# Kernel tuning notes

Measured on AMD Instinct MI355X. Metric: run time of the kernel, lower is better.

Reference implementation:

```python
import jax, jax.numpy as jnp
import numpy as np
from jax import lax

ITER_TIME = 32
DECAY = 0.9


def setup_inputs() -> dict:
    key = jax.random.key(0)
    k1, k2, k3, k4 = jax.random.split(key, 4)
    B, D_in, N, D_out = 256, 1024, 4096, 256
    s_in = 1.0 / np.sqrt(D_in)
    s_rec = 0.5 / np.sqrt(N)  # keep recurrence stable
    s_out = 1.0 / np.sqrt(N)
    return {
        "x": jax.random.normal(k1, (B, D_in), dtype=jnp.float32),
        "W_i": jax.random.normal(k2, (D_in, N), dtype=jnp.float32) * s_in,
        "b": jnp.zeros((N,), dtype=jnp.float32),
        "W_r": jax.random.normal(k3, (N, N), dtype=jnp.float32) * s_rec,
        "W_f": jax.random.normal(k4, (N, D_out), dtype=jnp.float32) * s_out,
    }


def reference(x, W_i, b, W_r, W_f):
    # prep_input_endure: constant input drive each timestep
    i_ = x @ W_i + b  # [B, N]
    u0 = jnp.zeros_like(i_)
    r0 = jnp.zeros_like(i_)

    def step(carry, _):
        u, r = carry
        u_new = DECAY * u + i_ + r           # leaky integration of drive + recurrent feedback
        a = jax.nn.relu(u_new)               # firing rate / surrogate spike
        r_new = a @ W_r                      # recurrent N->N feedback
        f = a @ W_f                          # readout N->Y
        return (u_new, r_new), (f, u_new)

    (_, _), (fs, us) = lax.scan(step, (u0, r0), None, length=ITER_TIME)
    output = jnp.transpose(fs, (1, 0, 2))  # [B, T, output_num]
    act = jnp.transpose(us, (1, 0, 2))     # [B, T, N_num]
    return output, act
```

## Files before the change

kernel.cpp:

```cpp
#include <hip/hip_runtime.h>
#include <hip/hip_bf16.h>

#define ITER_TIME 32
#define DECAY 0.9f

typedef __attribute__((ext_vector_type(8))) short short8;
typedef __attribute__((ext_vector_type(4))) float f32x4;
typedef __attribute__((ext_vector_type(4))) short short4v;
typedef unsigned short ushort_t;
typedef unsigned int u32;

__device__ __forceinline__ void gload16(const ushort_t* g, ushort_t* l) {
    __builtin_amdgcn_global_load_lds(
        (const __attribute__((address_space(1))) u32*)g,
        (__attribute__((address_space(3))) u32*)l, 16, 0, 0);
}

__global__ void conv_f32_bf16(const float* __restrict__ in,
                              __hip_bfloat16* __restrict__ out, int n) {
    int i = blockIdx.x * 256 + threadIdx.x;
    if (i < n) out[i] = __float2bfloat16(in[i]);
}

__global__ void transpose_f32_bf16(const float* __restrict__ in,
                                   __hip_bfloat16* __restrict__ out, int R,
                                   int C) {
    __shared__ float tile[32][33];
    int tx = threadIdx.x, ty = threadIdx.y;
    size_t x = blockIdx.x * 32 + tx;
    size_t y = blockIdx.y * 32 + ty;
    tile[ty][tx] = in[y * C + x];
    __syncthreads();
    size_t ox = blockIdx.y * 32 + tx;
    size_t oy = blockIdx.x * 32 + ty;
    out[oy * R + ox] = __float2bfloat16(tile[tx][ty]);
}

__global__ __launch_bounds__(256)
void gemm_splitk(const ushort_t* __restrict__ A,
                 const ushort_t* __restrict__ BT,
                 const ushort_t* __restrict__ BT2,
                 float* __restrict__ Cp,
                 float* __restrict__ C2p,
                 int K, int klen, int Nmain, int N2) {
    const int M = 256;
    __shared__ __attribute__((aligned(16))) ushort_t As[2][128 * 64];
    __shared__ __attribute__((aligned(16))) ushort_t Bs[2][128 * 64];

    int m0 = blockIdx.x * 128;
    int by = blockIdx.y;
    int ks = blockIdx.z;
    int ntile_main = Nmain >> 7;
    bool isB2 = (by >= ntile_main);
    const ushort_t* Bsrc = isB2 ? BT2 + (size_t)((by - ntile_main) * 128) * K
                                : BT + (size_t)(by * 128) * K;

    int t = threadIdx.x;
    int wave = t >> 6, lane = t & 63;
    int quad = lane >> 4, l16 = lane & 15;
    int wm = (wave >> 1) * 64, wn = (wave & 1) * 64;

    int lr = lane >> 3;
    int lcol = ((lane & 7) ^ lr) << 3;
    const ushort_t* aBase = A + (size_t)(m0 + wave * 32 + lr) * K + lcol;
    const ushort_t* bBase = Bsrc + (size_t)(wave * 32 + lr) * K + lcol;

    f32x4 acc[4][4];
#pragma unroll
    for (int i = 0; i < 4; i++)
#pragma unroll
        for (int j = 0; j < 4; j++) acc[i][j] = (f32x4){0.f, 0.f, 0.f, 0.f};

    int k0 = ks * klen;
    int nt = klen >> 6;

    int swz = (l16 & 7) << 3;

    auto stage = [&](int buf, int kk) {
#pragma unroll
        for (int i = 0; i < 4; ++i) {
            gload16(aBase + (size_t)(i * 8) * K + kk,
                    &As[buf][(wave * 4 + i) * 512]);
            gload16(bBase + (size_t)(i * 8) * K + kk,
                    &Bs[buf][(wave * 4 + i) * 512]);
        }
    };

    stage(0, k0);
    __syncthreads();
    int cur = 0;
    for (int it = 0; it < nt; ++it) {
        if (it + 1 < nt) stage(cur ^ 1, k0 + (it + 1) * 64);
#pragma unroll
        for (int kstep = 0; kstep < 2; ++kstep) {
            int ko = kstep * 32 + quad * 8;
            int pc = ko ^ swz;
            short8 af[4], bfr[4];
#pragma unroll
            for (int i = 0; i < 4; i++)
                af[i] = *(const short8*)&As[cur][(wm + i * 16 + l16) * 64 + pc];
#pragma unroll
            for (int j = 0; j < 4; j++)
                bfr[j] = *(const short8*)&Bs[cur][(wn + j * 16 + l16) * 64 + pc];
#pragma unroll
            for (int i = 0; i < 4; i++)
#pragma unroll
                for (int j = 0; j < 4; j++)
                    acc[i][j] = __builtin_amdgcn_mfma_f32_16x16x32_bf16(
                        af[i], bfr[j], acc[i][j], 0, 0, 0);
        }
        __syncthreads();
        cur ^= 1;
    }

#pragma unroll
    for (int i = 0; i < 4; i++) {
#pragma unroll
        for (int j = 0; j < 4; j++) {
            int gcol = by * 128 + wn + j * 16 + l16;
#pragma unroll
            for (int rr = 0; rr < 4; ++rr) {
                int grow = m0 + wm + i * 16 + quad * 4 + rr;
                float v = acc[i][j][rr];
                if (!isB2) {
                    Cp[(size_t)ks * M * Nmain + (size_t)grow * Nmain + gcol] = v;
                } else {
                    int c2 = gcol - Nmain;
                    C2p[(size_t)ks * M * N2 + (size_t)grow * N2 + c2] = v;
                }
            }
        }
    }
}

__global__ void elem_step(float* __restrict__ i_, float* __restrict__ u,
                          __hip_bfloat16* __restrict__ a,
                          const float* __restrict__ rp,
                          const float* __restrict__ fp,
                          const float* __restrict__ bias,
                          float* __restrict__ out, float* __restrict__ act,
                          int t, int KS) {
    int id4 = blockIdx.x * 256 + threadIdx.x;
    const int NU = 256 * 4096;
    const int NU4 = NU / 4;
    if (id4 < NU4) {
        if (t >= ITER_TIME) return;
        int id = id4 * 4;
        int b = id >> 12, n = id & 4095;
        f32x4 un;
        if (t == 0) {
            f32x4 iv = *(f32x4*)&i_[id] + *(const f32x4*)&bias[n];
            *(f32x4*)&i_[id] = iv;
            un = iv;
        } else {
            f32x4 s = *(f32x4*)&i_[id];
            for (int k = 0; k < KS; ++k)
                s += *(const f32x4*)&rp[(size_t)k * NU + id];
            un = DECAY * *(f32x4*)&u[id] + s;
        }
        *(f32x4*)&u[id] = un;
        short4v av;
#pragma unroll
        for (int j = 0; j < 4; ++j) {
            float ar = un[j] > 0.f ? un[j] : 0.f;
            __hip_bfloat16 h = __float2bfloat16(ar);
            av[j] = *(short*)&h;
        }
        *(short4v*)&a[id] = av;
        *(f32x4*)&act[(size_t)b * (ITER_TIME * 4096) + (size_t)t * 4096 + n] =
            un;
    } else {
        if (t == 0) return;
        int id2 = (id4 - NU4) * 4;
        const int NF = 256 * 256;
        int b = id2 >> 8, d = id2 & 255;
        f32x4 fv = {0.f, 0.f, 0.f, 0.f};
        for (int k = 0; k < KS; ++k)
            fv += *(const f32x4*)&fp[(size_t)k * NF + id2];
        *(f32x4*)&out[(size_t)b * (ITER_TIME * 256) + (size_t)(t - 1) * 256 +
                      d] = fv;
    }
}

extern "C" void kernel_launch(void* const* d_in, const int* in_sizes, int n_in,
                              void* d_out, int out_size, void* d_ws,
                              size_t ws_size, hipStream_t stream) {
    const float* x = (const float*)d_in[0];
    const float* Wi = (const float*)d_in[1];
    const float* bb = (const float*)d_in[2];
    const float* Wr = (const float*)d_in[3];
    const float* Wf = (const float*)d_in[4];

    float* out = (float*)d_out;
    float* act = out + (size_t)256 * ITER_TIME * 256;

    int KS = 8;
    if (ws_size < (size_t)0x4E80000) KS = 4;

    char* ws = (char*)d_ws;
    float* i_ = (float*)(ws + 0x0);
    float* u = (float*)(ws + 0x400000);
    __hip_bfloat16* a = (__hip_bfloat16*)(ws + 0x800000);
    size_t off = 0xA00000;
    float* rp = (float*)(ws + off);
    off += (size_t)KS << 22;
    float* fp = (float*)(ws + off);
    off += (size_t)KS << 18;
    __hip_bfloat16* WrT = (__hip_bfloat16*)(ws + off);
    off += 0x2000000;
    __hip_bfloat16* WfT = (__hip_bfloat16*)(ws + off);
    off += 0x200000;
    __hip_bfloat16* xb = (__hip_bfloat16*)(ws + off);
    __hip_bfloat16* WiT = (__hip_bfloat16*)(ws + 0xA00000);

    conv_f32_bf16<<<1024, 256, 0, stream>>>(x, xb, 256 * 1024);
    dim3 tb(32, 32);
    transpose_f32_bf16<<<dim3(128, 32), tb, 0, stream>>>(Wi, WiT, 1024, 4096);
    transpose_f32_bf16<<<dim3(128, 128), tb, 0, stream>>>(Wr, WrT, 4096, 4096);
    transpose_f32_bf16<<<dim3(8, 128), tb, 0, stream>>>(Wf, WfT, 4096, 256);

    gemm_splitk<<<dim3(2, 32, 1), 256, 0, stream>>>(
        (const ushort_t*)xb, (const ushort_t*)WiT, nullptr, i_, nullptr, 1024,
        1024, 4096, 256);

    int klen = 4096 / KS;
    for (int t = 0; t <= ITER_TIME; ++t) {
        elem_step<<<1088, 256, 0, stream>>>(i_, u, a, rp, fp, bb, out, act, t,
                                            KS);
        if (t < ITER_TIME) {
            gemm_splitk<<<dim3(2, 34, KS), 256, 0, stream>>>(
                (const ushort_t*)a, (const ushort_t*)WrT,
                (const ushort_t*)WfT, rp, fp, 4096, klen, 4096, 256);
        }
    }
}
```

Measured before the change: 1.337 ms.

## Fuse recurrent timestep loop into one persistent kernel with grid barriers

Replaces the 65 per-timestep launches of the elementwise and split-K GEMM kernels with a single persistent kernel of 272 blocks. The blocks alternate the elementwise update and the GEMM tiles, separated by atomic-counter grid barriers. Split-K is fixed at 4, and the act/out stores become nontemporal. This removes launch overhead and inter-kernel gaps, but relies on all 272 blocks being co-resident (otherwise it deadlocks) and adds spin-wait barrier cost.

```diff
diff --git a/kernel.cpp b/kernel.cpp
--- a/kernel.cpp
+++ b/kernel.cpp
@@ -3,6 +3,8 @@
 
 #define ITER_TIME 32
 #define DECAY 0.9f
+#define KS 4
+#define NBLK 272
 
 typedef __attribute__((ext_vector_type(8))) short short8;
 typedef __attribute__((ext_vector_type(4))) float f32x4;
@@ -17,7 +19,9 @@
 }
 
 __global__ void conv_f32_bf16(const float* __restrict__ in,
-                              __hip_bfloat16* __restrict__ out, int n) {
+                              __hip_bfloat16* __restrict__ out, int n,
+                              int* __restrict__ bar) {
+    if (blockIdx.x == 0 && threadIdx.x == 0) *bar = 0;
     int i = blockIdx.x * 256 + threadIdx.x;
     if (i < n) out[i] = __float2bfloat16(in[i]);
 }
@@ -37,23 +41,16 @@
 }
 
 __global__ __launch_bounds__(256)
-void gemm_splitk(const ushort_t* __restrict__ A,
-                 const ushort_t* __restrict__ BT,
-                 const ushort_t* __restrict__ BT2,
-                 float* __restrict__ Cp,
-                 float* __restrict__ C2p,
-                 int K, int klen, int Nmain, int N2) {
-    const int M = 256;
+void gemm_wi(const ushort_t* __restrict__ A,
+             const ushort_t* __restrict__ BT,
+             float* __restrict__ C,
+             int K, int Nmain) {
     __shared__ __attribute__((aligned(16))) ushort_t As[2][128 * 64];
     __shared__ __attribute__((aligned(16))) ushort_t Bs[2][128 * 64];
 
     int m0 = blockIdx.x * 128;
     int by = blockIdx.y;
-    int ks = blockIdx.z;
-    int ntile_main = Nmain >> 7;
-    bool isB2 = (by >= ntile_main);
-    const ushort_t* Bsrc = isB2 ? BT2 + (size_t)((by - ntile_main) * 128) * K
-                                : BT + (size_t)(by * 128) * K;
+    const ushort_t* Bsrc = BT + (size_t)(by * 128) * K;
 
     int t = threadIdx.x;
     int wave = t >> 6, lane = t & 63;
@@ -71,9 +68,7 @@
 #pragma unroll
         for (int j = 0; j < 4; j++) acc[i][j] = (f32x4){0.f, 0.f, 0.f, 0.f};
 
-    int k0 = ks * klen;
-    int nt = klen >> 6;
-
+    int nt = K >> 6;
     int swz = (l16 & 7) << 3;
 
     auto stage = [&](int buf, int kk) {
@@ -86,11 +81,11 @@
         }
     };
 
-    stage(0, k0);
+    stage(0, 0);
     __syncthreads();
     int cur = 0;
     for (int it = 0; it < nt; ++it) {
-        if (it + 1 < nt) stage(cur ^ 1, k0 + (it + 1) * 64);
+        if (it + 1 < nt) stage(cur ^ 1, (it + 1) * 64);
 #pragma unroll
         for (int kstep = 0; kstep < 2; ++kstep) {
             int ko = kstep * 32 + quad * 8;
@@ -114,7 +109,163 @@
     }
 
 #pragma unroll
-    for (int i = 0; i < 4; i++) {
+    for (int i = 0; i < 4; i++)
+#pragma unroll
+        for (int j = 0; j < 4; j++) {
+            int gcol = by * 128 + wn + j * 16 + l16;
+#pragma unroll
+            for (int rr = 0; rr < 4; ++rr) {
+                int grow = m0 + wm + i * 16 + quad * 4 + rr;
+                C[(size_t)grow * Nmain + gcol] = acc[i][j][rr];
+            }
+        }
+}
+
+__device__ __forceinline__ void grid_bar(int* bar, int phase) {
+    __syncthreads();
+    if (threadIdx.x == 0) {
+        __threadfence();
+        __hip_atomic_fetch_add(bar, 1, __ATOMIC_RELEASE,
+                               __HIP_MEMORY_SCOPE_AGENT);
+        int target = NBLK * (phase + 1);
+        while (__hip_atomic_load(bar, __ATOMIC_ACQUIRE,
+                                 __HIP_MEMORY_SCOPE_AGENT) < target)
+            __builtin_amdgcn_s_sleep(2);
+    }
+    __syncthreads();
+}
+
+__device__ __forceinline__ void elem_work(int t, float* __restrict__ i_,
+                                          float* __restrict__ u,
+                                          ushort_t* __restrict__ a,
+                                          const float* __restrict__ rp,
+                                          const float* __restrict__ fp,
+                                          const float* __restrict__ bias,
+                                          float* __restrict__ out,
+                                          float* __restrict__ act) {
+    const int NU = 256 * 4096, NU4 = NU / 4;
+    const int NF = 256 * 256, NF4 = NF / 4;
+    int gtid = blockIdx.x * 256 + threadIdx.x;
+    for (int id4 = gtid; id4 < NU4 + NF4; id4 += NBLK * 256) {
+        if (id4 < NU4) {
+            if (t >= ITER_TIME) continue;
+            int id = id4 * 4;
+            int b = id >> 12, n = id & 4095;
+            f32x4 un;
+            if (t == 0) {
+                f32x4 iv = *(f32x4*)&i_[id] + *(const f32x4*)&bias[n];
+                *(f32x4*)&i_[id] = iv;
+                un = iv;
+            } else {
+                f32x4 s = *(const f32x4*)&i_[id];
+#pragma unroll
+                for (int k = 0; k < KS; ++k)
+                    s += *(const f32x4*)&rp[(size_t)k * NU + id];
+                un = DECAY * *(f32x4*)&u[id] + s;
+            }
+            *(f32x4*)&u[id] = un;
+            short4v av;
+#pragma unroll
+            for (int j = 0; j < 4; ++j) {
+                float ar = un[j] > 0.f ? un[j] : 0.f;
+                __hip_bfloat16 h = __float2bfloat16(ar);
+                av[j] = *(short*)&h;
+            }
+            *(short4v*)&a[id] = av;
+            __builtin_nontemporal_store(
+                un, (f32x4*)&act[(size_t)b * (ITER_TIME * 4096) +
+                                 (size_t)t * 4096 + n]);
+        } else {
+            if (t == 0) continue;
+            int id2 = (id4 - NU4) * 4;
+            int b = id2 >> 8, d = id2 & 255;
+            f32x4 fv = {0.f, 0.f, 0.f, 0.f};
+#pragma unroll
+            for (int k = 0; k < KS; ++k)
+                fv += *(const f32x4*)&fp[(size_t)k * NF + id2];
+            __builtin_nontemporal_store(
+                fv, (f32x4*)&out[(size_t)b * (ITER_TIME * 256) +
+                                 (size_t)(t - 1) * 256 + d]);
+        }
+    }
+}
+
+__device__ __forceinline__ void gemm_tile(int blk, const ushort_t* __restrict__ A,
+                                          const ushort_t* __restrict__ WrT,
+                                          const ushort_t* __restrict__ WfT,
+                                          float* __restrict__ rp,
+                                          float* __restrict__ fp,
+                                          ushort_t* __restrict__ AsB,
+                                          ushort_t* __restrict__ BsB) {
+    const int K = 4096, klen = K / KS, Nmain = 4096, N2 = 256, M = 256;
+    int rem = blk % 68, ks = blk / 68;
+    int mt = rem & 1, by = rem >> 1;
+    int m0 = mt * 128;
+    bool isB2 = (by >= 32);
+    const ushort_t* Bsrc = isB2 ? WfT + (size_t)((by - 32) * 128) * K
+                                : WrT + (size_t)(by * 128) * K;
+
+    int t = threadIdx.x;
+    int wave = t >> 6, lane = t & 63;
+    int quad = lane >> 4, l16 = lane & 15;
+    int wm = (wave >> 1) * 64, wn = (wave & 1) * 64;
+
+    int lr = lane >> 3;
+    int lcol = ((lane & 7) ^ lr) << 3;
+    const ushort_t* aBase = A + (size_t)(m0 + wave * 32 + lr) * K + lcol;
+    const ushort_t* bBase = Bsrc + (size_t)(wave * 32 + lr) * K + lcol;
+
+    f32x4 acc[4][4];
+#pragma unroll
+    for (int i = 0; i < 4; i++)
+#pragma unroll
+        for (int j = 0; j < 4; j++) acc[i][j] = (f32x4){0.f, 0.f, 0.f, 0.f};
+
+    int k0 = ks * klen;
+    const int nt = klen >> 6;
+    int swz = (l16 & 7) << 3;
+
+    auto stage = [&](int buf, int kk) {
+#pragma unroll
+        for (int i = 0; i < 4; ++i) {
+            gload16(aBase + (size_t)(i * 8) * K + kk,
+                    &AsB[buf * 8192 + (wave * 4 + i) * 512]);
+            gload16(bBase + (size_t)(i * 8) * K + kk,
+                    &BsB[buf * 8192 + (wave * 4 + i) * 512]);
+        }
+    };
+
+    stage(0, k0);
+    __syncthreads();
+    int cur = 0;
+    for (int it = 0; it < nt; ++it) {
+        if (it + 1 < nt) stage(cur ^ 1, k0 + (it + 1) * 64);
+#pragma unroll
+        for (int kstep = 0; kstep < 2; ++kstep) {
+            int ko = kstep * 32 + quad * 8;
+            int pc = ko ^ swz;
+            short8 af[4], bfr[4];
+#pragma unroll
+            for (int i = 0; i < 4; i++)
+                af[i] = *(const short8*)&AsB[cur * 8192 +
+                                             (wm + i * 16 + l16) * 64 + pc];
+#pragma unroll
+            for (int j = 0; j < 4; j++)
+                bfr[j] = *(const short8*)&BsB[cur * 8192 +
+                                              (wn + j * 16 + l16) * 64 + pc];
+#pragma unroll
+            for (int i = 0; i < 4; i++)
+#pragma unroll
+                for (int j = 0; j < 4; j++)
+                    acc[i][j] = __builtin_amdgcn_mfma_f32_16x16x32_bf16(
+                        af[i], bfr[j], acc[i][j], 0, 0, 0);
+        }
+        __syncthreads();
+        cur ^= 1;
+    }
+
+#pragma unroll
+    for (int i = 0; i < 4; i++)
 #pragma unroll
         for (int j = 0; j < 4; j++) {
             int gcol = by * 128 + wn + j * 16 + l16;
@@ -123,63 +274,33 @@
                 int grow = m0 + wm + i * 16 + quad * 4 + rr;
                 float v = acc[i][j][rr];
                 if (!isB2) {
-                    Cp[(size_t)ks * M * Nmain + (size_t)grow * Nmain + gcol] = v;
+                    rp[(size_t)ks * M * Nmain + (size_t)grow * Nmain + gcol] = v;
                 } else {
                     int c2 = gcol - Nmain;
-                    C2p[(size_t)ks * M * N2 + (size_t)grow * N2 + c2] = v;
+                    fp[(size_t)ks * M * N2 + (size_t)grow * N2 + c2] = v;
                 }
             }
         }
-    }
-}
-
-__global__ void elem_step(float* __restrict__ i_, float* __restrict__ u,
-                          __hip_bfloat16* __restrict__ a,
-                          const float* __restrict__ rp,
-                          const float* __restrict__ fp,
-                          const float* __restrict__ bias,
-                          float* __restrict__ out, float* __restrict__ act,
-                          int t, int KS) {
-    int id4 = blockIdx.x * 256 + threadIdx.x;
-    const int NU = 256 * 4096;
-    const int NU4 = NU / 4;
-    if (id4 < NU4) {
-        if (t >= ITER_TIME) return;
-        int id = id4 * 4;
-        int b = id >> 12, n = id & 4095;
-        f32x4 un;
-        if (t == 0) {
-            f32x4 iv = *(f32x4*)&i_[id] + *(const f32x4*)&bias[n];
-            *(f32x4*)&i_[id] = iv;
-            un = iv;
-        } else {
-            f32x4 s = *(f32x4*)&i_[id];
-            for (int k = 0; k < KS; ++k)
-                s += *(const f32x4*)&rp[(size_t)k * NU + id];
-            un = DECAY * *(f32x4*)&u[id] + s;
-        }
-        *(f32x4*)&u[id] = un;
-        short4v av;
-#pragma unroll
-        for (int j = 0; j < 4; ++j) {
-            float ar = un[j] > 0.f ? un[j] : 0.f;
-            __hip_bfloat16 h = __float2bfloat16(ar);
-            av[j] = *(short*)&h;
-        }
-        *(short4v*)&a[id] = av;
-        *(f32x4*)&act[(size_t)b * (ITER_TIME * 4096) + (size_t)t * 4096 + n] =
-            un;
-    } else {
-        if (t == 0) return;
-        int id2 = (id4 - NU4) * 4;
-        const int NF = 256 * 256;
-        int b = id2 >> 8, d = id2 & 255;
-        f32x4 fv = {0.f, 0.f, 0.f, 0.f};
-        for (int k = 0; k < KS; ++k)
-            fv += *(const f32x4*)&fp[(size_t)k * NF + id2];
-        *(f32x4*)&out[(size_t)b * (ITER_TIME * 256) + (size_t)(t - 1) * 256 +
-                      d] = fv;
-    }
+}
+
+__global__ __launch_bounds__(256, 2)
+void persist(ushort_t* __restrict__ a, const ushort_t* __restrict__ WrT,
+             const ushort_t* __restrict__ WfT, float* __restrict__ i_,
+             float* __restrict__ u, float* __restrict__ rp,
+             float* __restrict__ fp, const float* __restrict__ bias,
+             float* __restrict__ out, float* __restrict__ act,
+             int* __restrict__ bar) {
+    __shared__ __attribute__((aligned(16))) ushort_t As[2 * 8192];
+    __shared__ __attribute__((aligned(16))) ushort_t Bs[2 * 8192];
+    int blk = blockIdx.x;
+    int phase = 0;
+    for (int t = 0; t < ITER_TIME; ++t) {
+        elem_work(t, i_, u, a, rp, fp, bias, out, act);
+        grid_bar(bar, phase++);
+        gemm_tile(blk, a, WrT, WfT, rp, fp, As, Bs);
+        grid_bar(bar, phase++);
+    }
+    elem_work(ITER_TIME, i_, u, a, rp, fp, bias, out, act);
 }
 
 extern "C" void kernel_launch(void* const* d_in, const int* in_sizes, int n_in,
@@ -194,43 +315,29 @@
     float* out = (float*)d_out;
     float* act = out + (size_t)256 * ITER_TIME * 256;
 
-    int KS = 8;
-    if (ws_size < (size_t)0x4E80000) KS = 4;
-
     char* ws = (char*)d_ws;
     float* i_ = (float*)(ws + 0x0);
     float* u = (float*)(ws + 0x400000);
     __hip_bfloat16* a = (__hip_bfloat16*)(ws + 0x800000);
-    size_t off = 0xA00000;
-    float* rp = (float*)(ws + off);
-    off += (size_t)KS << 22;
-    float* fp = (float*)(ws + off);
-    off += (size_t)KS << 18;
-    __hip_bfloat16* WrT = (__hip_bfloat16*)(ws + off);
-    off += 0x2000000;
-    __hip_bfloat16* WfT = (__hip_bfloat16*)(ws + off);
-    off += 0x200000;
-    __hip_bfloat16* xb = (__hip_bfloat16*)(ws + off);
+    float* rp = (float*)(ws + 0xA00000);
+    float* fp = (float*)(ws + 0x1A00000);
+    __hip_bfloat16* WrT = (__hip_bfloat16*)(ws + 0x1B00000);
+    __hip_bfloat16* WfT = (__hip_bfloat16*)(ws + 0x3B00000);
+    __hip_bfloat16* xb = (__hip_bfloat16*)(ws + 0x3D00000);
+    int* bar = (int*)(ws + 0x3D80000);
     __hip_bfloat16* WiT = (__hip_bfloat16*)(ws + 0xA00000);
 
-    conv_f32_bf16<<<1024, 256, 0, stream>>>(x, xb, 256 * 1024);
+    conv_f32_bf16<<<1024, 256, 0, stream>>>(x, xb, 256 * 1024, bar);
     dim3 tb(32, 32);
     transpose_f32_bf16<<<dim3(128, 32), tb, 0, stream>>>(Wi, WiT, 1024, 4096);
     transpose_f32_bf16<<<dim3(128, 128), tb, 0, stream>>>(Wr, WrT, 4096, 4096);
     transpose_f32_bf16<<<dim3(8, 128), tb, 0, stream>>>(Wf, WfT, 4096, 256);
 
-    gemm_splitk<<<dim3(2, 32, 1), 256, 0, stream>>>(
-        (const ushort_t*)xb, (const ushort_t*)WiT, nullptr, i_, nullptr, 1024,
-        1024, 4096, 256);
-
-    int klen = 4096 / KS;
-    for (int t = 0; t <= ITER_TIME; ++t) {
-        elem_step<<<1088, 256, 0, stream>>>(i_, u, a, rp, fp, bb, out, act, t,
-                                            KS);
-        if (t < ITER_TIME) {
-            gemm_splitk<<<dim3(2, 34, KS), 256, 0, stream>>>(
-                (const ushort_t*)a, (const ushort_t*)WrT,
-                (const ushort_t*)WfT, rp, fp, 4096, klen, 4096, 256);
-        }
-    }
-}
+    gemm_wi<<<dim3(2, 32), 256, 0, stream>>>((const ushort_t*)xb,
+                                             (const ushort_t*)WiT, i_, 1024,
+                                             4096);
+
+    persist<<<NBLK, 256, 0, stream>>>(
+        (ushort_t*)a, (const ushort_t*)WrT, (const ushort_t*)WfT, i_, u, rp,
+        fp, bb, out, act, bar);
+}
```

After: 4.167 ms. 3.12x slower.

## Retile recurrent GEMM to 128x32 tiles with 2-way split-K and fuse init epilogue

Applied to the files above, without the earlier changes.

Replaces the 128x128-tile, 8-way split-K recurrent GEMM with a 128x32-tile kernel using 2-way split-K over 544 blocks. Block indices are remapped so tiles land evenly across the XCDs. This cuts partial-sum traffic and the reduction work in the elementwise step. The input projection GEMM now writes the bias-added drive, u, a0 and act[0] directly in its epilogue, which removes the t=0 elementwise pass. The last step runs only the readout columns, and output stores use nontemporal hints. Smaller tiles lower per-block arithmetic intensity and reload the A operand more often.

```diff
diff --git a/kernel.cpp b/kernel.cpp
--- a/kernel.cpp
+++ b/kernel.cpp
@@ -37,23 +37,17 @@
 }
 
 __global__ __launch_bounds__(256)
-void gemm_splitk(const ushort_t* __restrict__ A,
-                 const ushort_t* __restrict__ BT,
-                 const ushort_t* __restrict__ BT2,
-                 float* __restrict__ Cp,
-                 float* __restrict__ C2p,
-                 int K, int klen, int Nmain, int N2) {
-    const int M = 256;
+void gemm_wi(const ushort_t* __restrict__ A,
+             const ushort_t* __restrict__ BT,
+             const float* __restrict__ bias, float* __restrict__ i_,
+             float* __restrict__ u, __hip_bfloat16* __restrict__ a0,
+             float* __restrict__ act, int K) {
     __shared__ __attribute__((aligned(16))) ushort_t As[2][128 * 64];
     __shared__ __attribute__((aligned(16))) ushort_t Bs[2][128 * 64];
 
     int m0 = blockIdx.x * 128;
     int by = blockIdx.y;
-    int ks = blockIdx.z;
-    int ntile_main = Nmain >> 7;
-    bool isB2 = (by >= ntile_main);
-    const ushort_t* Bsrc = isB2 ? BT2 + (size_t)((by - ntile_main) * 128) * K
-                                : BT + (size_t)(by * 128) * K;
+    const ushort_t* Bsrc = BT + (size_t)by * 128 * K;
 
     int t = threadIdx.x;
     int wave = t >> 6, lane = t & 63;
@@ -71,9 +65,7 @@
 #pragma unroll
         for (int j = 0; j < 4; j++) acc[i][j] = (f32x4){0.f, 0.f, 0.f, 0.f};
 
-    int k0 = ks * klen;
-    int nt = klen >> 6;
-
+    int nt = K >> 6;
     int swz = (l16 & 7) << 3;
 
     auto stage = [&](int buf, int kk) {
@@ -86,6 +78,108 @@
         }
     };
 
+    stage(0, 0);
+    __syncthreads();
+    int cur = 0;
+    for (int it = 0; it < nt; ++it) {
+        if (it + 1 < nt) stage(cur ^ 1, (it + 1) * 64);
+#pragma unroll
+        for (int kstep = 0; kstep < 2; ++kstep) {
+            int ko = kstep * 32 + quad * 8;
+            int pc = ko ^ swz;
+            short8 af[4], bfr[4];
+#pragma unroll
+            for (int i = 0; i < 4; i++)
+                af[i] = *(const short8*)&As[cur][(wm + i * 16 + l16) * 64 + pc];
+#pragma unroll
+            for (int j = 0; j < 4; j++)
+                bfr[j] = *(const short8*)&Bs[cur][(wn + j * 16 + l16) * 64 + pc];
+#pragma unroll
+            for (int i = 0; i < 4; i++)
+#pragma unroll
+                for (int j = 0; j < 4; j++)
+                    acc[i][j] = __builtin_amdgcn_mfma_f32_16x16x32_bf16(
+                        af[i], bfr[j], acc[i][j], 0, 0, 0);
+        }
+        __syncthreads();
+        cur ^= 1;
+    }
+
+#pragma unroll
+    for (int i = 0; i < 4; i++)
+#pragma unroll
+        for (int j = 0; j < 4; j++) {
+            int gcol = by * 128 + wn + j * 16 + l16;
+#pragma unroll
+            for (int rr = 0; rr < 4; ++rr) {
+                int grow = m0 + wm + i * 16 + quad * 4 + rr;
+                size_t p = (size_t)grow * 4096 + gcol;
+                float iv = acc[i][j][rr] + bias[gcol];
+                i_[p] = iv;
+                u[p] = iv;
+                __builtin_nontemporal_store(
+                    iv, &act[(size_t)grow * (ITER_TIME * 4096) + gcol]);
+                float ar = iv > 0.f ? iv : 0.f;
+                a0[p] = __float2bfloat16(ar);
+            }
+        }
+}
+
+template <int ONLY_F>
+__global__ __launch_bounds__(256)
+void gemm_step(const ushort_t* __restrict__ A,
+               const ushort_t* __restrict__ BT,
+               float* __restrict__ rp,
+               float* __restrict__ fp) {
+    const int K = 4096, klen = 2048;
+    __shared__ __attribute__((aligned(16))) ushort_t As[2][128 * 64];
+    __shared__ __attribute__((aligned(16))) ushort_t Bs[2][32 * 64];
+
+    int blk = blockIdx.x;
+    int by, ks, m;
+    if (ONLY_F) {
+        by = 128 + (blk >> 2);
+        int w = blk & 3;
+        m = w & 1;
+        ks = w >> 1;
+    } else {
+        int x = blk & 15, g = blk >> 4;
+        int xcd = x & 7;
+        m = x >> 3;
+        int pair = g * 8 + xcd;
+        by = pair % 136;
+        ks = pair / 136;
+    }
+    int m0 = m * 128;
+    const ushort_t* Bsrc = BT + (size_t)by * 32 * K;
+
+    int tid = threadIdx.x;
+    int wave = tid >> 6, lane = tid & 63;
+    int quad = lane >> 4, l16 = lane & 15;
+
+    int lr = lane >> 3;
+    int lcol = ((lane & 7) ^ lr) << 3;
+    const ushort_t* aBase = A + (size_t)(m0 + wave * 32 + lr) * K + lcol;
+    const ushort_t* bBase = Bsrc + (size_t)(wave * 8 + lr) * K + lcol;
+
+    f32x4 acc[2][2];
+#pragma unroll
+    for (int i = 0; i < 2; i++)
+#pragma unroll
+        for (int j = 0; j < 2; j++) acc[i][j] = (f32x4){0.f, 0.f, 0.f, 0.f};
+
+    const int k0 = ks * klen;
+    const int nt = klen >> 6;
+    int swz = (l16 & 7) << 3;
+
+    auto stage = [&](int buf, int kk) {
+#pragma unroll
+        for (int i = 0; i < 4; ++i)
+            gload16(aBase + (size_t)(i * 8) * K + kk,
+                    &As[buf][(wave * 4 + i) * 512]);
+        gload16(bBase + kk, &Bs[buf][wave * 512]);
+    };
+
     stage(0, k0);
     __syncthreads();
     int cur = 0;
@@ -95,17 +189,18 @@
         for (int kstep = 0; kstep < 2; ++kstep) {
             int ko = kstep * 32 + quad * 8;
             int pc = ko ^ swz;
-            short8 af[4], bfr[4];
-#pragma unroll
-            for (int i = 0; i < 4; i++)
-                af[i] = *(const short8*)&As[cur][(wm + i * 16 + l16) * 64 + pc];
-#pragma unroll
-            for (int j = 0; j < 4; j++)
-                bfr[j] = *(const short8*)&Bs[cur][(wn + j * 16 + l16) * 64 + pc];
-#pragma unroll
-            for (int i = 0; i < 4; i++)
-#pragma unroll
-                for (int j = 0; j < 4; j++)
+            short8 af[2], bfr[2];
+#pragma unroll
+            for (int i = 0; i < 2; i++)
+                af[i] = *(const short8*)&As[cur][(wave * 32 + i * 16 + l16) * 64 +
+                                                 pc];
+#pragma unroll
+            for (int j = 0; j < 2; j++)
+                bfr[j] = *(const short8*)&Bs[cur][(j * 16 + l16) * 64 + pc];
+#pragma unroll
+            for (int i = 0; i < 2; i++)
+#pragma unroll
+                for (int j = 0; j < 2; j++)
                     acc[i][j] = __builtin_amdgcn_mfma_f32_16x16x32_bf16(
                         af[i], bfr[j], acc[i][j], 0, 0, 0);
         }
@@ -114,50 +209,42 @@
     }
 
 #pragma unroll
-    for (int i = 0; i < 4; i++) {
-#pragma unroll
-        for (int j = 0; j < 4; j++) {
-            int gcol = by * 128 + wn + j * 16 + l16;
+    for (int i = 0; i < 2; i++)
+#pragma unroll
+        for (int j = 0; j < 2; j++) {
+            int cl = j * 16 + l16;
 #pragma unroll
             for (int rr = 0; rr < 4; ++rr) {
-                int grow = m0 + wm + i * 16 + quad * 4 + rr;
+                int grow = m0 + wave * 32 + i * 16 + quad * 4 + rr;
                 float v = acc[i][j][rr];
-                if (!isB2) {
-                    Cp[(size_t)ks * M * Nmain + (size_t)grow * Nmain + gcol] = v;
+                if (by < 128) {
+                    rp[(size_t)ks * (256 * 4096) + (size_t)grow * 4096 +
+                       by * 32 + cl] = v;
                 } else {
-                    int c2 = gcol - Nmain;
-                    C2p[(size_t)ks * M * N2 + (size_t)grow * N2 + c2] = v;
+                    fp[(size_t)ks * (256 * 256) + (size_t)grow * 256 +
+                       (by - 128) * 32 + cl] = v;
                 }
             }
         }
-    }
-}
-
-__global__ void elem_step(float* __restrict__ i_, float* __restrict__ u,
+}
+
+__global__ void elem_step(const float* __restrict__ i_, float* __restrict__ u,
                           __hip_bfloat16* __restrict__ a,
                           const float* __restrict__ rp,
                           const float* __restrict__ fp,
-                          const float* __restrict__ bias,
                           float* __restrict__ out, float* __restrict__ act,
-                          int t, int KS) {
-    int id4 = blockIdx.x * 256 + threadIdx.x;
-    const int NU = 256 * 4096;
-    const int NU4 = NU / 4;
+                          int t, int fonly) {
+    const int NU = 256 * 4096, NU4 = NU / 4;
+    const int NF = 256 * 256, NF4 = NF / 4;
+    int raw = blockIdx.x * 256 + threadIdx.x;
+    int id4 = fonly ? (NU4 + raw) : raw;
+    if (id4 >= NU4 + NF4) return;
     if (id4 < NU4) {
-        if (t >= ITER_TIME) return;
         int id = id4 * 4;
         int b = id >> 12, n = id & 4095;
-        f32x4 un;
-        if (t == 0) {
-            f32x4 iv = *(f32x4*)&i_[id] + *(const f32x4*)&bias[n];
-            *(f32x4*)&i_[id] = iv;
-            un = iv;
-        } else {
-            f32x4 s = *(f32x4*)&i_[id];
-            for (int k = 0; k < KS; ++k)
-                s += *(const f32x4*)&rp[(size_t)k * NU + id];
-            un = DECAY * *(f32x4*)&u[id] + s;
-        }
+        f32x4 s = *(const f32x4*)&i_[id] + *(const f32x4*)&rp[id] +
+                  *(const f32x4*)&rp[NU + id];
+        f32x4 un = DECAY * *(const f32x4*)&u[id] + s;
         *(f32x4*)&u[id] = un;
         short4v av;
 #pragma unroll
@@ -167,18 +254,16 @@
             av[j] = *(short*)&h;
         }
         *(short4v*)&a[id] = av;
-        *(f32x4*)&act[(size_t)b * (ITER_TIME * 4096) + (size_t)t * 4096 + n] =
-            un;
+        __builtin_nontemporal_store(
+            un, (f32x4*)&act[(size_t)b * (ITER_TIME * 4096) +
+                             (size_t)t * 4096 + n]);
     } else {
-        if (t == 0) return;
         int id2 = (id4 - NU4) * 4;
-        const int NF = 256 * 256;
         int b = id2 >> 8, d = id2 & 255;
-        f32x4 fv = {0.f, 0.f, 0.f, 0.f};
-        for (int k = 0; k < KS; ++k)
-            fv += *(const f32x4*)&fp[(size_t)k * NF + id2];
-        *(f32x4*)&out[(size_t)b * (ITER_TIME * 256) + (size_t)(t - 1) * 256 +
-                      d] = fv;
+        f32x4 fv = *(const f32x4*)&fp[id2] + *(const f32x4*)&fp[NF + id2];
+        __builtin_nontemporal_store(
+            fv, (f32x4*)&out[(size_t)b * (ITER_TIME * 256) +
+                             (size_t)(t - 1) * 256 + d]);
     }
 }
 
@@ -194,43 +279,35 @@
     float* out = (float*)d_out;
     float* act = out + (size_t)256 * ITER_TIME * 256;
 
-    int KS = 8;
-    if (ws_size < (size_t)0x4E80000) KS = 4;
-
     char* ws = (char*)d_ws;
-    float* i_ = (float*)(ws + 0x0);
-    float* u = (float*)(ws + 0x400000);
-    __hip_bfloat16* a = (__hip_bfloat16*)(ws + 0x800000);
-    size_t off = 0xA00000;
-    float* rp = (float*)(ws + off);
-    off += (size_t)KS << 22;
-    float* fp = (float*)(ws + off);
-    off += (size_t)KS << 18;
-    __hip_bfloat16* WrT = (__hip_bfloat16*)(ws + off);
-    off += 0x2000000;
-    __hip_bfloat16* WfT = (__hip_bfloat16*)(ws + off);
-    off += 0x200000;
-    __hip_bfloat16* xb = (__hip_bfloat16*)(ws + off);
-    __hip_bfloat16* WiT = (__hip_bfloat16*)(ws + 0xA00000);
+    __hip_bfloat16* BT = (__hip_bfloat16*)(ws + 0x0);
+    float* i_ = (float*)(ws + 0x2200000);
+    float* u = (float*)(ws + 0x2600000);
+    __hip_bfloat16* a = (__hip_bfloat16*)(ws + 0x2A00000);
+    float* rp = (float*)(ws + 0x2C00000);
+    float* fp = (float*)(ws + 0x3400000);
+    __hip_bfloat16* xb = (__hip_bfloat16*)(ws + 0x3480000);
+    __hip_bfloat16* WiT = (__hip_bfloat16*)(ws + 0x3500000);
 
     conv_f32_bf16<<<1024, 256, 0, stream>>>(x, xb, 256 * 1024);
     dim3 tb(32, 32);
     transpose_f32_bf16<<<dim3(128, 32), tb, 0, stream>>>(Wi, WiT, 1024, 4096);
-    transpose_f32_bf16<<<dim3(128, 128), tb, 0, stream>>>(Wr, WrT, 4096, 4096);
-    transpose_f32_bf16<<<dim3(8, 128), tb, 0, stream>>>(Wf, WfT, 4096, 256);
-
-    gemm_splitk<<<dim3(2, 32, 1), 256, 0, stream>>>(
-        (const ushort_t*)xb, (const ushort_t*)WiT, nullptr, i_, nullptr, 1024,
-        1024, 4096, 256);
-
-    int klen = 4096 / KS;
-    for (int t = 0; t <= ITER_TIME; ++t) {
-        elem_step<<<1088, 256, 0, stream>>>(i_, u, a, rp, fp, bb, out, act, t,
-                                            KS);
-        if (t < ITER_TIME) {
-            gemm_splitk<<<dim3(2, 34, KS), 256, 0, stream>>>(
-                (const ushort_t*)a, (const ushort_t*)WrT,
-                (const ushort_t*)WfT, rp, fp, 4096, klen, 4096, 256);
-        }
-    }
-}
+    transpose_f32_bf16<<<dim3(128, 128), tb, 0, stream>>>(Wr, BT, 4096, 4096);
+    transpose_f32_bf16<<<dim3(8, 128), tb, 0, stream>>>(
+        Wf, BT + (size_t)4096 * 4096, 4096, 256);
+
+    gemm_wi<<<dim3(2, 32), 256, 0, stream>>>((const ushort_t*)xb,
+                                             (const ushort_t*)WiT, bb, i_, u,
+                                             a, act, 1024);
+
+    for (int t = 0; t < ITER_TIME - 1; ++t) {
+        gemm_step<0><<<544, 256, 0, stream>>>((const ushort_t*)a,
+                                              (const ushort_t*)BT, rp, fp);
+        elem_step<<<1088, 256, 0, stream>>>(i_, u, a, rp, fp, out, act, t + 1,
+                                            0);
+    }
+    gemm_step<1><<<32, 256, 0, stream>>>((const ushort_t*)a,
+                                         (const ushort_t*)BT, rp, fp);
+    elem_step<<<64, 256, 0, stream>>>(i_, u, a, rp, fp, out, act, ITER_TIME,
+                                      1);
+}
```

Result: faster. 1.218 ms (-8.9%).
